# Kernel optimization log

Measured on AMD Instinct MI355X. Metric: run time of the kernel, lower is better.

Reference implementation:

```python
import jax, jax.numpy as jnp
import numpy as np
import math

H, D = 8, 128            # num_heads, head_dim (hidden=1024)
CHUNK, PAST, FUT = 12, 12, 0
CTX = CHUNK + PAST + FUT  # 24
SOFTCAP = 50.0
INVALID = 1e-09
Q_SCALE = D ** (-0.5) / math.log(2)
K_SCALE = math.log(1.0 + math.e) / math.log(2)


def setup_inputs() -> dict:
    key = jax.random.key(0)
    ks = jax.random.split(key, 7)
    B, S, HS = 16, 2400, 1024
    w = lambda k: jax.random.normal(k, (HS, HS), jnp.float32) * 0.02
    return {
        "x": jax.random.normal(ks[0], (B, S, HS), jnp.float32),
        "pos_emb": jax.random.normal(ks[1], (CTX + 1, HS), jnp.float32),
        "Wq": w(ks[2]),
        "Wk": w(ks[3]),
        "Wv": w(ks[4]),
        "Wpost": w(ks[5]),
        "Wrel": w(ks[6]),
        "per_dim_scale": jnp.zeros((D,), jnp.float32),
    }


def _to_blocks(t):
    # [B,S,H,D] -> [B,nb,CHUNK,H,D] (pad S up to multiple of CHUNK)
    B, S, h, d = t.shape
    nb = -(-S // CHUNK)
    t = jnp.pad(t, ((0, 0), (0, nb * CHUNK - S), (0, 0), (0, 0)))
    return t.reshape(B, nb, CHUNK, h, d)


def _block_context(t):
    # [B,S,H,D] -> [B,nb,CTX,H,D]: per-block window of PAST left context + chunk + FUT
    B, S, h, d = t.shape
    nb = -(-S // CHUNK)
    tp = jnp.pad(t, ((0, 0), (PAST, FUT + CHUNK - 1), (0, 0), (0, 0)))
    idx = jnp.arange(nb)[:, None] * CHUNK + jnp.arange(CTX)[None, :]  # [nb,CTX]
    return tp[:, idx]  # gather -> [B,nb,CTX,H,D]


def _rel_shift(x):
    # [B,H,nb,CHUNK,P] -> [B,H,nb,CHUNK,CTX] via Transformer-XL reshape trick
    B, h, nb, bs, P = x.shape
    x = jnp.pad(x, ((0, 0), (0, 0), (0, 0), (0, 0), (0, CTX + 1 - P)))
    x = x.reshape(B, h, nb, bs * (CTX + 1))[..., : bs * CTX]
    return x.reshape(B, h, nb, bs, CTX)


def reference(x, pos_emb, Wq, Wk, Wv, Wpost, Wrel, per_dim_scale):
    B, S, HS = x.shape
    q = (x @ Wq).reshape(B, S, H, D) * Q_SCALE * jax.nn.softplus(per_dim_scale)
    k = (x @ Wk).reshape(B, S, H, D) * K_SCALE
    v = (x @ Wv).reshape(B, S, H, D)

    qb = _to_blocks(q)        # [B,nb,CHUNK,H,D]
    kc = _block_context(k)    # [B,nb,CTX,H,D]
    vc = _block_context(v)    # [B,nb,CTX,H,D]
    nb = qb.shape[1]

    rel_k = (pos_emb @ Wrel).reshape(-1, H, D)  # [P,H,D]

    # content-content scores: [B,H,nb,CHUNK,CTX]
    matrix_ac = jnp.einsum('bnqhd,bnkhd->bhnqk', qb, kc)
    # content-position scores with rel-shift: [B,H,nb,CHUNK,P] -> [...,CTX]
    matrix_bd = jnp.einsum('bnqhd,phd->bhnqp', qb, rel_k)
    matrix_bd = _rel_shift(matrix_bd)

    attn = jnp.tanh((matrix_ac + matrix_bd) / SOFTCAP) * SOFTCAP
    attn = jax.nn.softmax(attn, axis=-1)

    out = jnp.einsum('bhnqk,bnkhd->bnqhd', attn, vc)  # [B,nb,CHUNK,H,D]
    out = out.reshape(B, nb * CHUNK, H * D)[:, :S, :]
    return out @ Wpost
```

## Files before the change

### kernel.cpp

```cpp
#include <hip/hip_runtime.h>
#include <hip/hip_bf16.h>
#include <cmath>

#define AS_GLOBAL __attribute__((address_space(1)))
#define AS_LDS    __attribute__((address_space(3)))

typedef __attribute__((ext_vector_type(8))) short bf16x8;
typedef __attribute__((ext_vector_type(4))) float f32x4;
typedef unsigned short u16;

__device__ __forceinline__ u16 f2bf(float f) {
  union { __hip_bfloat16 h; u16 u; } cv;
  cv.h = __float2bfloat16(f);
  return cv.u;
}
__device__ __forceinline__ float bf2f(u16 u) {
  union { unsigned u32; float f; } v;
  v.u32 = ((unsigned)u) << 16;
  return v.f;
}


__global__ void k_f32_to_bf16(const float* __restrict__ in, u16* __restrict__ out, int n4) {
  int i = blockIdx.x * 256 + threadIdx.x;
  if (i >= n4) return;
  float4 v = ((const float4*)in)[i];
  ushort4 o;
  o.x = f2bf(v.x); o.y = f2bf(v.y); o.z = f2bf(v.z); o.w = f2bf(v.w);
  ((ushort4*)out)[i] = o;
}

__global__ void k_transpose_w(const float* __restrict__ in, u16* __restrict__ out) {
  __shared__ float tile[32][33];
  const int tx = threadIdx.x & 31;
  const int ty = threadIdx.x >> 5;
  const int x0 = blockIdx.x * 32, y0 = blockIdx.y * 32;
  #pragma unroll
  for (int i = 0; i < 32; i += 8)
    tile[ty + i][tx] = in[(size_t)(y0 + ty + i) * 1024 + x0 + tx];
  __syncthreads();
  #pragma unroll
  for (int i = 0; i < 32; i += 8)
    out[(size_t)(x0 + ty + i) * 1024 + y0 + tx] = f2bf(tile[tx][ty + i]);
}

__global__ void k_qscale(const float* __restrict__ pds, float* __restrict__ qs, float qscale_c) {
  int n = blockIdx.x * 256 + threadIdx.x;
  float s = pds[n & 127];
  qs[n] = qscale_c * log1pf(expf(s));
}

__global__ void k_relk(const float* __restrict__ pos, const u16* __restrict__ wrt,
                       u16* __restrict__ relkb) {
  __shared__ float prow[1024];
  const int tid = threadIdx.x;
  const int p = blockIdx.y;
  ((float4*)prow)[tid] = ((const float4*)(pos + (size_t)p * 1024))[tid];
  __syncthreads();
  int nn = blockIdx.x * 256 + tid;
  const u16* wr = wrt + (size_t)nn * 1024;
  float acc = 0.f;
  for (int kk = 0; kk < 1024; kk += 8) {
    ushort4 u0 = *(const ushort4*)(wr + kk);
    ushort4 u1 = *(const ushort4*)(wr + kk + 4);
    acc += bf2f(u0.x) * prow[kk + 0] + bf2f(u0.y) * prow[kk + 1]
         + bf2f(u0.z) * prow[kk + 2] + bf2f(u0.w) * prow[kk + 3]
         + bf2f(u1.x) * prow[kk + 4] + bf2f(u1.y) * prow[kk + 5]
         + bf2f(u1.z) * prow[kk + 6] + bf2f(u1.w) * prow[kk + 7];
  }
  relkb[(size_t)p * 1024 + nn] = f2bf(acc);
}

template <int OUTMODE>
__global__ __launch_bounds__(256) void k_gemm_bt(
    const u16* __restrict__ A, const u16* __restrict__ Bt, void* __restrict__ Cout,
    const float* __restrict__ scale_vec, float scale_scalar, int M, int N, int K) {
  __shared__ __align__(16) u16 As[128 * 32];
  __shared__ __align__(16) u16 Bs[128 * 32];
  const int tid = threadIdx.x;
  const int wave = tid >> 6, lane = tid & 63;
  const int quad = lane >> 4, l16 = lane & 15;
  const int wm = wave >> 1, wn = wave & 1;
  const int m0 = blockIdx.y * 128, n0 = blockIdx.x * 128;

  f32x4 acc[4][4];
  #pragma unroll
  for (int i = 0; i < 4; ++i)
    #pragma unroll
    for (int j = 0; j < 4; ++j) {
      f32x4 z = {0.f, 0.f, 0.f, 0.f};
      acc[i][j] = z;
    }

  for (int k0 = 0; k0 < K; k0 += 32) {
    __syncthreads();
    #pragma unroll
    for (int i = 0; i < 2; ++i) {
      int cbase = i * 256 + wave * 64;
      int c = cbase + lane;
      const u16* ga = A + (size_t)(m0 + (c >> 2)) * K + (k0 + (c & 3) * 8);
      __builtin_amdgcn_global_load_lds((const AS_GLOBAL u16*)ga, (AS_LDS u16*)&As[cbase * 8], 16, 0, 0);
      const u16* gb = Bt + (size_t)(n0 + (c >> 2)) * K + (k0 + (c & 3) * 8);
      __builtin_amdgcn_global_load_lds((const AS_GLOBAL u16*)gb, (AS_LDS u16*)&Bs[cbase * 8], 16, 0, 0);
    }
    __syncthreads();

    bf16x8 af[4], bfr[4];
    #pragma unroll
    for (int mi = 0; mi < 4; ++mi)
      af[mi] = *(const bf16x8*)&As[(wm * 64 + mi * 16 + l16) * 32 + quad * 8];
    #pragma unroll
    for (int ni = 0; ni < 4; ++ni)
      bfr[ni] = *(const bf16x8*)&Bs[(wn * 64 + ni * 16 + l16) * 32 + quad * 8];
    #pragma unroll
    for (int mi = 0; mi < 4; ++mi)
      #pragma unroll
      for (int ni = 0; ni < 4; ++ni)
        acc[mi][ni] = __builtin_amdgcn_mfma_f32_16x16x32_bf16(af[mi], bfr[ni], acc[mi][ni], 0, 0, 0);
  }

  if (OUTMODE == 2) {
    #pragma unroll
    for (int ni = 0; ni < 4; ++ni) {
      int col = n0 + wn * 64 + ni * 16 + l16;
      #pragma unroll
      for (int mi = 0; mi < 4; ++mi) {
        int row = m0 + wm * 64 + mi * 16 + quad * 4;
        ushort4 o;
        o.x = f2bf(acc[mi][ni][0]);
        o.y = f2bf(acc[mi][ni][1]);
        o.z = f2bf(acc[mi][ni][2]);
        o.w = f2bf(acc[mi][ni][3]);
        *(ushort4*)&((u16*)Cout)[(size_t)col * M + row] = o;
      }
    }
  } else {
    #pragma unroll
    for (int ni = 0; ni < 4; ++ni) {
      int col = n0 + wn * 64 + ni * 16 + l16;
      float cs = scale_vec ? scale_vec[col] : scale_scalar;
      #pragma unroll
      for (int mi = 0; mi < 4; ++mi) {
        int row = m0 + wm * 64 + mi * 16 + quad * 4;
        #pragma unroll
        for (int r = 0; r < 4; ++r) {
          float v = acc[mi][ni][r] * cs;
          if (OUTMODE == 1)
            ((u16*)Cout)[(size_t)(row + r) * N + col] = f2bf(v);
          else
            ((float*)Cout)[(size_t)(row + r) * N + col] = v;
        }
      }
    }
  }
}

__global__ __launch_bounds__(256) void k_attn_mfma(
    const u16* __restrict__ q, const u16* __restrict__ k, const u16* __restrict__ vt,
    const u16* __restrict__ relkb, u16* __restrict__ ctx) {
  __shared__ float bdm_s[4][400];
  __shared__ u16 attnb[4][16 * 32];

  const int tid = threadIdx.x;
  const int w = tid >> 6, lane = tid & 63;
  const int l16 = lane & 15, quad = lane >> 4;
  const int id = blockIdx.x * 4 + w;
  const int b = id / 1600;
  const int rr = id % 1600;
  const int n = rr >> 3, h = rr & 7;
  const int s0 = n * 12;
  const size_t rowbase = (size_t)b * 2400;

  bf16x8 qf[4];
  {
    int sq = s0 + l16;
    if (sq > 2399) sq = 2399;
    const u16* qp = q + ((rowbase + sq) * 1024 + (size_t)h * 128 + quad * 8);
    #pragma unroll
    for (int c = 0; c < 4; ++c) qf[c] = *(const bf16x8*)(qp + 32 * c);
  }

  #pragma unroll
  for (int pt = 0; pt < 2; ++pt) {
    int p = pt * 16 + l16;
    const u16* rp = relkb + ((size_t)p * 1024 + (size_t)h * 128 + quad * 8);
    f32x4 acc = {0.f, 0.f, 0.f, 0.f};
    #pragma unroll
    for (int c = 0; c < 4; ++c)
      acc = __builtin_amdgcn_mfma_f32_16x16x32_bf16(qf[c], *(const bf16x8*)(rp + 32 * c), acc, 0, 0, 0);
    if (p < 25) {
      #pragma unroll
      for (int r = 0; r < 4; ++r)
        bdm_s[w][(quad * 4 + r) * 25 + p] = acc[r];
    }
  }
  __threadfence_block();

  float l0[4], l1[4];
  #pragma unroll
  for (int kt = 0; kt < 2; ++kt) {
    int t = kt * 16 + l16;
    int sk = s0 - 12 + t;
    bool kvalid = ((unsigned)sk < 2400u);
    int ska = kvalid ? sk : 0;
    const u16* kp = k + ((rowbase + ska) * 1024 + (size_t)h * 128 + quad * 8);
    short km = kvalid ? (short)0xFFFF : (short)0;
    bf16x8 kmv = {km, km, km, km, km, km, km, km};
    f32x4 acc = {0.f, 0.f, 0.f, 0.f};
    #pragma unroll
    for (int c = 0; c < 4; ++c) {
      bf16x8 kf = *(const bf16x8*)(kp + 32 * c);
      kf &= kmv;
      acc = __builtin_amdgcn_mfma_f32_16x16x32_bf16(qf[c], kf, acc, 0, 0, 0);
    }
    #pragma unroll
    for (int r = 0; r < 4; ++r) {
      float bd = bdm_s[w][(quad * 4 + r) * 24 + t];
      float lg = tanhf((acc[r] + bd) * (1.0f / 50.0f)) * 50.0f;
      if (kt == 1 && l16 >= 8) lg = -INFINITY;
      if (kt) l1[r] = lg; else l0[r] = lg;
    }
  }

  float at0[4], at1[4];
  #pragma unroll
  for (int r = 0; r < 4; ++r) {
    float m = fmaxf(l0[r], l1[r]);
    #pragma unroll
    for (int s = 1; s < 16; s <<= 1) m = fmaxf(m, __shfl_xor(m, s, 64));
    float e0 = __expf(l0[r] - m), e1 = __expf(l1[r] - m);
    float sum = e0 + e1;
    #pragma unroll
    for (int s = 1; s < 16; s <<= 1) sum += __shfl_xor(sum, s, 64);
    float inv = 1.0f / sum;
    at0[r] = e0 * inv;
    at1[r] = e1 * inv;
  }

  #pragma unroll
  for (int r = 0; r < 4; ++r) {
    attnb[w][(quad * 4 + r) * 32 + l16] = f2bf(at0[r]);
    attnb[w][(quad * 4 + r) * 32 + 16 + l16] = f2bf(at1[r]);
  }
  __threadfence_block();
  bf16x8 af = *(const bf16x8*)&attnb[w][l16 * 32 + quad * 8];

  int slo = s0 - 12 + quad * 8;
  bf16x8 vmsk;
  #pragma unroll
  for (int j = 0; j < 8; ++j)
    vmsk[j] = ((unsigned)(slo + j) < 2400u) ? (short)0xFFFF : (short)0;

  f32x4 oacc[8];
  #pragma unroll
  for (int dt = 0; dt < 8; ++dt) {
    int col = h * 128 + dt * 16 + l16;
    const u16* vp = vt + ((size_t)col * 38400 + (long)(rowbase + s0 - 12 + quad * 8));
    ushort4 va = *(const ushort4*)vp;
    ushort4 vb = *(const ushort4*)(vp + 4);
    bf16x8 vf = {(short)va.x, (short)va.y, (short)va.z, (short)va.w,
                 (short)vb.x, (short)vb.y, (short)vb.z, (short)vb.w};
    vf &= vmsk;
    f32x4 z = {0.f, 0.f, 0.f, 0.f};
    oacc[dt] = __builtin_amdgcn_mfma_f32_16x16x32_bf16(af, vf, z, 0, 0, 0);
  }

  if (quad < 3) {
    #pragma unroll
    for (int dt = 0; dt < 8; ++dt) {
      int col = h * 128 + dt * 16 + l16;
      #pragma unroll
      for (int r = 0; r < 4; ++r) {
        int qi = quad * 4 + r;
        ctx[(rowbase + s0 + qi) * 1024 + col] = f2bf(oacc[dt][r]);
      }
    }
  }
}


extern "C" void kernel_launch(void* const* d_in, const int* in_sizes, int n_in,
                              void* d_out, int out_size, void* d_ws, size_t ws_size,
                              hipStream_t stream) {
  const float* x       = (const float*)d_in[0];
  const float* pos_emb = (const float*)d_in[1];
  const float* Wq      = (const float*)d_in[2];
  const float* Wk      = (const float*)d_in[3];
  const float* Wv      = (const float*)d_in[4];
  const float* Wpost   = (const float*)d_in[5];
  const float* Wrel    = (const float*)d_in[6];
  const float* pds     = (const float*)d_in[7];
  float* out = (float*)d_out;

  const int M = 38400, HS = 1024;
  const size_t XE = (size_t)M * HS;

  u16* xbf = (u16*)d_ws;
  u16* qbf = xbf + XE;
  u16* kbf = qbf + XE;
  u16* vt_alloc = kbf + XE;
  u16* vt = vt_alloc + 16;
  u16* wqt = vt_alloc + XE + 64;
  u16* wkt = wqt + (size_t)HS * HS;
  u16* wvt = wkt + (size_t)HS * HS;
  u16* wrt = wvt + (size_t)HS * HS;
  u16* wpt = wrt + (size_t)HS * HS;
  u16* relkb = wpt + (size_t)HS * HS;
  float* qsc = (float*)(relkb + 32 * 1024);

  const double LN2 = 0.6931471805599453;
  const float QS = (float)((1.0 / sqrt(128.0)) / LN2);
  const float KS = (float)(log(1.0 + exp(1.0)) / LN2);

  k_f32_to_bf16<<<(int)(XE / 4 / 256), 256, 0, stream>>>(x, xbf, (int)(XE / 4));
  dim3 tg(32, 32);
  k_transpose_w<<<tg, 256, 0, stream>>>(Wq, wqt);
  k_transpose_w<<<tg, 256, 0, stream>>>(Wk, wkt);
  k_transpose_w<<<tg, 256, 0, stream>>>(Wv, wvt);
  k_transpose_w<<<tg, 256, 0, stream>>>(Wrel, wrt);
  k_transpose_w<<<tg, 256, 0, stream>>>(Wpost, wpt);
  k_qscale<<<4, 256, 0, stream>>>(pds, qsc, QS);
  k_relk<<<dim3(4, 25), 256, 0, stream>>>(pos_emb, wrt, relkb);
  dim3 gg(HS / 128, M / 128);
  k_gemm_bt<1><<<gg, 256, 0, stream>>>(xbf, wqt, qbf, qsc, 1.0f, M, HS, HS);
  k_gemm_bt<1><<<gg, 256, 0, stream>>>(xbf, wkt, kbf, nullptr, KS, M, HS, HS);
  k_gemm_bt<2><<<gg, 256, 0, stream>>>(xbf, wvt, vt, nullptr, 1.0f, M, HS, HS);
  k_attn_mfma<<<25600 / 4, 256, 0, stream>>>(qbf, kbf, vt, relkb, xbf);
  k_gemm_bt<0><<<gg, 256, 0, stream>>>(xbf, wpt, out, nullptr, 1.0f, M, HS, HS);
}
```

Baseline: 950.4 us.

## Replace GEMM with 256x256 tiled, double-buffered, swizzled-LDS MFMA kernel

Replaces the 128x128 single-buffered GEMM with a 256x256 tile kernel using 512 threads, a K-step of 64, and double-buffered LDS staging via global_load_lds with partial vmcnt waits. An XOR swizzle on LDS columns avoids bank conflicts, and a blockIdx remap groups workgroups for L2 locality. It also raises wave priority during MFMA. The aim is more data reuse per load and overlap of memory with compute in the four projection GEMMs. In exchange it uses more registers and 128KB of LDS per block, which limits occupancy, and it assumes M and N are multiples of 256 and the block count is a multiple of 8.

```diff
diff --git a/kernel.cpp b/kernel.cpp
--- a/kernel.cpp
+++ b/kernel.cpp
@@ -71,77 +71,128 @@
   relkb[(size_t)p * 1024 + nn] = f2bf(acc);
 }
 
+
+#define BAR() __builtin_amdgcn_s_barrier()
+#define VMCNT(n) asm volatile("s_waitcnt vmcnt(" #n ")" ::: "memory")
+
+#define STAGE(d, t)                                                                       \
+  do {                                                                                    \
+    const int koff_ = (t) << 6;                                                           \
+    _Pragma("unroll")                                                                     \
+    for (int j_ = 0; j_ < 4; ++j_) {                                                      \
+      int f_ = tid + j_ * 512;                                                            \
+      int r_ = f_ >> 3;                                                                   \
+      int cs_ = ((f_ & 7) ^ (r_ & 7)) << 3;                                               \
+      __builtin_amdgcn_global_load_lds(                                                   \
+          (const AS_GLOBAL u16*)(A + (size_t)(m0 + r_) * K + koff_ + cs_),                \
+          (AS_LDS u16*)&lds[d][0][f_ << 3], 16, 0, 0);                                    \
+      __builtin_amdgcn_global_load_lds(                                                   \
+          (const AS_GLOBAL u16*)(Bt + (size_t)(n0 + r_) * K + koff_ + cs_),               \
+          (AS_LDS u16*)&lds[d][1][f_ << 3], 16, 0, 0);                                    \
+    }                                                                                     \
+  } while (0)
+
+#define COMPUTE(d)                                                                        \
+  do {                                                                                    \
+    bf16x8 bfr_[4][2];                                                                    \
+    _Pragma("unroll")                                                                     \
+    for (int ni_ = 0; ni_ < 4; ++ni_) {                                                   \
+      int brow_ = wn * 64 + ni_ * 16 + l16;                                               \
+      int bb_ = brow_ * 64, bx_ = brow_ & 7;                                              \
+      bfr_[ni_][0] = *(const bf16x8*)&lds[d][1][bb_ + ((quad ^ bx_) << 3)];               \
+      bfr_[ni_][1] = *(const bf16x8*)&lds[d][1][bb_ + (((4 + quad) ^ bx_) << 3)];         \
+    }                                                                                     \
+    __builtin_amdgcn_s_setprio(1);                                                        \
+    _Pragma("unroll")                                                                     \
+    for (int mi_ = 0; mi_ < 8; ++mi_) {                                                   \
+      int arow_ = wm * 128 + mi_ * 16 + l16;                                              \
+      int ab_ = arow_ * 64, ax_ = arow_ & 7;                                              \
+      bf16x8 a0_ = *(const bf16x8*)&lds[d][0][ab_ + ((quad ^ ax_) << 3)];                 \
+      bf16x8 a1_ = *(const bf16x8*)&lds[d][0][ab_ + (((4 + quad) ^ ax_) << 3)];           \
+      _Pragma("unroll")                                                                   \
+      for (int ni_ = 0; ni_ < 4; ++ni_) {                                                 \
+        acc[mi_][ni_] =                                                                   \
+            __builtin_amdgcn_mfma_f32_16x16x32_bf16(a0_, bfr_[ni_][0], acc[mi_][ni_], 0, 0, 0); \
+        acc[mi_][ni_] =                                                                   \
+            __builtin_amdgcn_mfma_f32_16x16x32_bf16(a1_, bfr_[ni_][1], acc[mi_][ni_], 0, 0, 0); \
+      }                                                                                   \
+    }                                                                                     \
+    __builtin_amdgcn_s_setprio(0);                                                        \
+  } while (0)
+
 template <int OUTMODE>
-__global__ __launch_bounds__(256) void k_gemm_bt(
+__global__ __launch_bounds__(512, 2) void k_gemm256(
     const u16* __restrict__ A, const u16* __restrict__ Bt, void* __restrict__ Cout,
     const float* __restrict__ scale_vec, float scale_scalar, int M, int N, int K) {
-  __shared__ __align__(16) u16 As[128 * 32];
-  __shared__ __align__(16) u16 Bs[128 * 32];
+  __shared__ __align__(16) u16 lds[2][2][16384];
   const int tid = threadIdx.x;
   const int wave = tid >> 6, lane = tid & 63;
-  const int quad = lane >> 4, l16 = lane & 15;
-  const int wm = wave >> 1, wn = wave & 1;
-  const int m0 = blockIdx.y * 128, n0 = blockIdx.x * 128;
-
-  f32x4 acc[4][4];
-  #pragma unroll
-  for (int i = 0; i < 4; ++i)
+  const int l16 = lane & 15, quad = lane >> 4;
+  const int wm = wave >> 2, wn = wave & 3;
+
+  const int q8 = (int)gridDim.x >> 3;
+  const int wg = ((int)blockIdx.x & 7) * q8 + ((int)blockIdx.x >> 3);
+  const int ntn = N >> 8;
+  const int m0 = (wg / ntn) << 8;
+  const int n0 = (wg % ntn) << 8;
+
+  f32x4 acc[8][4];
+  #pragma unroll
+  for (int i = 0; i < 8; ++i)
     #pragma unroll
     for (int j = 0; j < 4; ++j) {
       f32x4 z = {0.f, 0.f, 0.f, 0.f};
       acc[i][j] = z;
     }
 
-  for (int k0 = 0; k0 < K; k0 += 32) {
-    __syncthreads();
-    #pragma unroll
-    for (int i = 0; i < 2; ++i) {
-      int cbase = i * 256 + wave * 64;
-      int c = cbase + lane;
-      const u16* ga = A + (size_t)(m0 + (c >> 2)) * K + (k0 + (c & 3) * 8);
-      __builtin_amdgcn_global_load_lds((const AS_GLOBAL u16*)ga, (AS_LDS u16*)&As[cbase * 8], 16, 0, 0);
-      const u16* gb = Bt + (size_t)(n0 + (c >> 2)) * K + (k0 + (c & 3) * 8);
-      __builtin_amdgcn_global_load_lds((const AS_GLOBAL u16*)gb, (AS_LDS u16*)&Bs[cbase * 8], 16, 0, 0);
-    }
-    __syncthreads();
-
-    bf16x8 af[4], bfr[4];
-    #pragma unroll
-    for (int mi = 0; mi < 4; ++mi)
-      af[mi] = *(const bf16x8*)&As[(wm * 64 + mi * 16 + l16) * 32 + quad * 8];
-    #pragma unroll
-    for (int ni = 0; ni < 4; ++ni)
-      bfr[ni] = *(const bf16x8*)&Bs[(wn * 64 + ni * 16 + l16) * 32 + quad * 8];
-    #pragma unroll
-    for (int mi = 0; mi < 4; ++mi)
+  STAGE(0, 0);
+  STAGE(1, 1);
+  VMCNT(8);
+  BAR();
+
+  const int nk = K >> 6;
+  for (int i = 0; i + 2 < nk; i += 2) {
+    COMPUTE(0);
+    BAR();
+    STAGE(0, i + 2);
+    VMCNT(8);
+    BAR();
+    COMPUTE(1);
+    BAR();
+    STAGE(1, i + 3);
+    VMCNT(8);
+    BAR();
+  }
+  COMPUTE(0);
+  VMCNT(0);
+  BAR();
+  COMPUTE(1);
+
+  const int mb = m0 + wm * 128, nb = n0 + wn * 64;
+  if (OUTMODE == 2) {
+    u16* C = (u16*)Cout;
+    #pragma unroll
+    for (int ni = 0; ni < 4; ++ni) {
+      int col = nb + ni * 16 + l16;
       #pragma unroll
-      for (int ni = 0; ni < 4; ++ni)
-        acc[mi][ni] = __builtin_amdgcn_mfma_f32_16x16x32_bf16(af[mi], bfr[ni], acc[mi][ni], 0, 0, 0);
-  }
-
-  if (OUTMODE == 2) {
-    #pragma unroll
-    for (int ni = 0; ni < 4; ++ni) {
-      int col = n0 + wn * 64 + ni * 16 + l16;
-      #pragma unroll
-      for (int mi = 0; mi < 4; ++mi) {
-        int row = m0 + wm * 64 + mi * 16 + quad * 4;
+      for (int mi = 0; mi < 8; ++mi) {
+        int row = mb + mi * 16 + quad * 4;
         ushort4 o;
         o.x = f2bf(acc[mi][ni][0]);
         o.y = f2bf(acc[mi][ni][1]);
         o.z = f2bf(acc[mi][ni][2]);
         o.w = f2bf(acc[mi][ni][3]);
-        *(ushort4*)&((u16*)Cout)[(size_t)col * M + row] = o;
+        *(ushort4*)&C[(size_t)col * M + row] = o;
       }
     }
   } else {
     #pragma unroll
     for (int ni = 0; ni < 4; ++ni) {
-      int col = n0 + wn * 64 + ni * 16 + l16;
+      int col = nb + ni * 16 + l16;
       float cs = scale_vec ? scale_vec[col] : scale_scalar;
       #pragma unroll
-      for (int mi = 0; mi < 4; ++mi) {
-        int row = m0 + wm * 64 + mi * 16 + quad * 4;
+      for (int mi = 0; mi < 8; ++mi) {
+        int row = mb + mi * 16 + quad * 4;
         #pragma unroll
         for (int r = 0; r < 4; ++r) {
           float v = acc[mi][ni][r] * cs;
@@ -321,10 +372,10 @@
   k_transpose_w<<<tg, 256, 0, stream>>>(Wpost, wpt);
   k_qscale<<<4, 256, 0, stream>>>(pds, qsc, QS);
   k_relk<<<dim3(4, 25), 256, 0, stream>>>(pos_emb, wrt, relkb);
-  dim3 gg(HS / 128, M / 128);
-  k_gemm_bt<1><<<gg, 256, 0, stream>>>(xbf, wqt, qbf, qsc, 1.0f, M, HS, HS);
-  k_gemm_bt<1><<<gg, 256, 0, stream>>>(xbf, wkt, kbf, nullptr, KS, M, HS, HS);
-  k_gemm_bt<2><<<gg, 256, 0, stream>>>(xbf, wvt, vt, nullptr, 1.0f, M, HS, HS);
+  const int NWG = (M / 256) * (HS / 256);
+  k_gemm256<1><<<NWG, 512, 0, stream>>>(xbf, wqt, qbf, qsc, 1.0f, M, HS, HS);
+  k_gemm256<1><<<NWG, 512, 0, stream>>>(xbf, wkt, kbf, nullptr, KS, M, HS, HS);
+  k_gemm256<2><<<NWG, 512, 0, stream>>>(xbf, wvt, vt, nullptr, 1.0f, M, HS, HS);
   k_attn_mfma<<<25600 / 4, 256, 0, stream>>>(qbf, kbf, vt, relkb, xbf);
-  k_gemm_bt<0><<<gg, 256, 0, stream>>>(xbf, wpt, out, nullptr, 1.0f, M, HS, HS);
-}
+  k_gemm256<0><<<NWG, 512, 0, stream>>>(xbf, wpt, out, nullptr, 1.0f, M, HS, HS);
+}
```

After: 880.0 us. -7.4%, faster.
